# Performance work log

Measured on AMD Instinct MI355X. Metric: run time of the kernel, lower is better.

The kernel has to match this reference:

```python
import jax, jax.numpy as jnp
import numpy as np

T, B, NS, NC = 64, 128, 64, 32
NSC = NS + NC


def setup_inputs() -> dict:
    key = jax.random.key(0)
    k0, k1, k2, k3, k4, k5 = jax.random.split(key, 6)
    # SPD quadratic cost: C = L L^T + I  (mpc.pytorch requires Quu > 0)
    L = 0.1 * jax.random.normal(k0, (T, B, NSC, NSC), jnp.float32)
    C = jnp.einsum('tbij,tbkj->tbik', L, L) + jnp.eye(NSC, dtype=jnp.float32)
    c = jax.random.normal(k1, (T, B, NSC), jnp.float32)
    # Stable linear dynamics: x+ = Fx x + Fu u + f
    Fx = 0.95 * jnp.eye(NS, dtype=jnp.float32) + 0.02 * jax.random.normal(k2, (T, B, NS, NS), jnp.float32)
    Fu = 0.1 * jax.random.normal(k3, (T, B, NS, NC), jnp.float32)
    F = jnp.concatenate([Fx, Fu], axis=-1)
    f = 0.1 * jax.random.normal(k4, (T, B, NS), jnp.float32)
    x_init = jax.random.normal(k5, (B, NS), jnp.float32)
    return {"C": C, "c": c, "F": F, "f": f, "x_init": x_init}


def _lqr(C, c, F, f, x_init):
    """Exact batched time-varying LQR (Riccati backward pass + rollout).

    This is the math of MPC.solve_lqr_subproblem for LinDx/QuadCost with no
    control bounds; with quadratic cost & linear dynamics one iLQR iteration
    (alpha=1) is the exact solution.
    Returns tau = [x; u] trajectory, shape [T, B, NS+NC].
    """
    n = x_init.shape[-1]
    b = x_init.shape[0]
    dt = C.dtype

    def bwd(carry, inp):
        V, v = carry                      # V: [B,n,n], v: [B,n]
        Ct, ct, Ft, ft = inp
        # Q = C + F^T V F ; q = c + F^T (V f + v)
        Q = Ct + jnp.einsum('bsi,bst,btj->bij', Ft, V, Ft)
        q = ct + jnp.einsum('bsi,bs->bi', Ft, v + jnp.einsum('bst,bt->bs', V, ft))
        Qxx, Qxu = Q[:, :n, :n], Q[:, :n, n:]
        Qux, Quu = Q[:, n:, :n], Q[:, n:, n:]
        qx, qu = q[:, :n], q[:, n:]
        # One solve for both feedback gain K and feedforward k
        Kk = -jnp.linalg.solve(Quu, jnp.concatenate([Qux, qu[..., None]], axis=-1))
        K, k = Kk[..., :n], Kk[..., n]    # K: [B,nc,n], k: [B,nc]
        Vn = (Qxx
              + jnp.einsum('bim,bmj->bij', Qxu, K)
              + jnp.einsum('bmi,bmj->bij', K, Qux)
              + jnp.einsum('bmi,bmn,bnj->bij', K, Quu, K))
        Vn = 0.5 * (Vn + jnp.swapaxes(Vn, -1, -2))
        vn = (qx
              + jnp.einsum('bim,bm->bi', Qxu, k)
              + jnp.einsum('bmi,bm->bi', K, qu + jnp.einsum('bmn,bn->bm', Quu, k)))
        return (Vn, vn), (K, k)

    V0 = jnp.zeros((b, n, n), dt)
    v0 = jnp.zeros((b, n), dt)
    _, (Ks, ks) = jax.lax.scan(bwd, (V0, v0), (C, c, F, f), reverse=True)

    def fwd(x, inp):
        K, k, Ft, ft = inp
        u = jnp.einsum('bmi,bi->bm', K, x) + k
        tau = jnp.concatenate([x, u], axis=-1)
        x_next = jnp.einsum('bsi,bi->bs', Ft, tau) + ft
        return x_next, tau

    _, taus = jax.lax.scan(fwd, x_init, (Ks, ks, F, f))
    return taus  # [T, B, NSC]


def reference(C, c, F, f, x_init):
    return _lqr(C, c, F, f, x_init)
```

## Files before the change

kernel.cpp:

```cpp
#include <hip/hip_runtime.h>


constexpr int T_   = 64;
constexpr int B_   = 128;
constexpr int NS_  = 64;
constexpr int NC_  = 32;
constexpr int NSC_ = 96;

constexpr int OFF_VS   = 0;
constexpr int OFF_WS   = 4352;
constexpr int OFF_QU   = 10752;
constexpr int OFF_SS   = 13952;
constexpr int OFF_LT   = 18304;
constexpr int OFF_INVD = 20416;
constexpr int OFF_QV   = 20480;
constexpr int OFF_HV   = 20580;
constexpr int OFF_VV   = 20644;
constexpr int OFF_FB   = 20776;
constexpr int OFF_CU   = 33064;
constexpr int OFF_CF   = 36136;
constexpr int SMEM_F   = 37160;

typedef __attribute__((address_space(3))) void*       lds_vp;
typedef const __attribute__((address_space(1))) void* gas_vp;

__device__ __forceinline__ void g2l16(const float* g, float* l) {
  __builtin_amdgcn_global_load_lds((gas_vp)g, (lds_vp)l, 16, 0, 0);
}

__device__ __forceinline__ float rdlane(float v, int l) {
  return __builtin_bit_cast(float, __builtin_amdgcn_readlane(__builtin_bit_cast(int, v), l));
}

#define ASM_WAIT(S) asm volatile("s_waitcnt " S ::: "memory")
#define BAR()       __builtin_amdgcn_s_barrier()

__global__ __launch_bounds__(512) void lqr_all(
    const float* __restrict__ Cg, const float* __restrict__ cvg,
    const float* __restrict__ Fg, const float* __restrict__ fvg,
    const float* __restrict__ x0g, float* __restrict__ outg,
    float* __restrict__ Sws)
{
  const int b    = blockIdx.x;
  const int tid  = threadIdx.x;
  const int wid  = tid >> 6;
  const int lane = tid & 63;

  __shared__ float smem[SMEM_F];
  float (*Vs)[68]  = (float(*)[68]) (smem + OFF_VS);
  float (*Ws)[100] = (float(*)[100])(smem + OFF_WS);
  float (*Qu)[100] = (float(*)[100])(smem + OFF_QU);
  float* qv = smem + OFF_QV;
  float* hv = smem + OFF_HV;
  float* vv = smem + OFF_VV;

  for (int e = tid; e < 4352; e += 512) smem[e] = 0.f;
  if (tid < 64) vv[tid] = 0.f;

  const int b_r4 = (tid & 15) * 4;
  const int b_c4 = (tid >> 4) * 4;
  const int q_i0 = (tid / 24) * 4;
  const int q_j0 = (tid % 24) * 4;
  const int tvs  = tid - 192;
  const int v_r  = (tvs & 15) * 4;
  const int v_c  = ((tvs >> 4) & 15) * 4;
  const int tf2  = tid - 256;
  const int f_i  = ((tf2 >> 4) & 15) * 4;
  const int f_j  = (tf2 & 15) * 4;

  auto backsolve2 = [&](int pb, size_t tbn) {
    const int c = (tid - 128) >> 1;
    const int h = (tid - 128) & 1;
    const float (*Sp)[68]  = (const float(*)[68])(smem + OFF_SS + pb * 2176);
    const float (*LTp)[33] = (const float(*)[33])(smem + OFF_LT + pb * 1056);
    const float* ivp = smem + OFF_INVD + pb * 32;
    float r[16];
#pragma unroll
    for (int m = 0; m < 16; ++m) r[m] = Sp[2 * m + h][c];
    float* Sg = Sws + tbn * 2080;
#pragma unroll
    for (int k = 31; k >= 0; --k) {
      const float cand  = r[k >> 1] * ivp[k];
      const float other = __shfl_xor(cand, 1);
      const float xk = ((k & 1) == h) ? cand : other;
      if ((k & 1) == h) Sg[k * 65 + c] = xk;
#pragma unroll
      for (int m = 0; m <= (k - 1) >> 1; ++m) {
        if (h < k - 2 * m)
          r[m] -= LTp[2 * m + h][k] * xk;
      }
    }
  };

  {
    const size_t tb0 = (size_t)(T_ - 1) * B_ + b;
    if (wid == 7) {
      const int o = lane * 4;
      g2l16(cvg + tb0 * 96 + (o < 96 ? o : 92), smem + OFF_CF);
      g2l16(fvg + tb0 * 64 + (o < 64 ? o : 60), smem + OFF_CF + 256);
    }
    const float* Fbase = Fg + tb0 * (NS_ * NSC_);
#pragma unroll
    for (int r = 0; r < 3; ++r) {
      const int q = wid * 3 + r;
      g2l16(Fbase + q * 256 + lane * 4, smem + OFF_FB + q * 256);
    }
  }

  int cur = 0;

  for (int t = T_ - 1; t >= 0; --t) {
    const size_t tb = (size_t)t * B_ + b;
    float4 cxa0 = {}, cxa1 = {}, cxb0 = {}, cxb1 = {};

    {
      if (wid < 3) {
        const float* CuB = Cg + tb * 9216 + 64 * 96;
#pragma unroll
        for (int r = 0; r < 4; ++r) {
          const int q = wid * 4 + r;
          g2l16(CuB + q * 256 + lane * 4, smem + OFF_CU + q * 256);
        }
      } else if (wid < 7) {
        const float* Cb = Cg + tb * 9216;
        cxa0 = *(const float4*)(Cb + (v_r + 0) * 96 + v_c);
        cxa1 = *(const float4*)(Cb + (v_r + 1) * 96 + v_c);
        cxb0 = *(const float4*)(Cb + (v_r + 2) * 96 + v_c);
        cxb1 = *(const float4*)(Cb + (v_r + 3) * 96 + v_c);
      }
      const int tp = (t > 0) ? (t - 1) : 0;
      const size_t tbp = (size_t)tp * B_ + b;
      if (wid == 7) {
        float* cdst = smem + OFF_CF + (cur ^ 1) * 512;
        const int o = lane * 4;
        g2l16(cvg + tbp * 96 + (o < 96 ? o : 92), cdst);
        g2l16(fvg + tbp * 64 + (o < 64 ? o : 60), cdst + 256);
      }
      const float* Fbase = Fg + tbp * (NS_ * NSC_);
      float* fdst = smem + OFF_FB + (cur ^ 1) * 6144;
#pragma unroll
      for (int r = 0; r < 3; ++r) {
        const int q = wid * 3 + r;
        g2l16(Fbase + q * 256 + lane * 4, fdst + q * 256);
      }
    }

    if (wid == 7) { ASM_WAIT("vmcnt(5) lgkmcnt(0)"); }
    else         { ASM_WAIT("vmcnt(7) lgkmcnt(0)"); }
    BAR();

    const float* Fb = smem + OFF_FB + cur * 6144;
    const float* cf = smem + OFF_CF + cur * 512;

    if (tid < 384) {
      float acc[4][4];
#pragma unroll
      for (int a2 = 0; a2 < 4; ++a2)
#pragma unroll
        for (int j = 0; j < 4; ++j) acc[a2][j] = 0.f;
#pragma unroll 4
      for (int u = 0; u < 64; ++u) {
        const float4 va = *(const float4*)&Vs[u][b_r4];
        const float4 fb = *(const float4*)(Fb + u * 96 + b_c4);
        const float av[4] = {va.x, va.y, va.z, va.w};
        const float bv[4] = {fb.x, fb.y, fb.z, fb.w};
#pragma unroll
        for (int a2 = 0; a2 < 4; ++a2)
#pragma unroll
          for (int j = 0; j < 4; ++j) acc[a2][j] += av[a2] * bv[j];
      }
#pragma unroll
      for (int a2 = 0; a2 < 4; ++a2)
        *(float4*)&Ws[b_r4 + a2][b_c4] =
            make_float4(acc[a2][0], acc[a2][1], acc[a2][2], acc[a2][3]);
    } else if (tid < 448) {
      const int s = tid - 384;
      float acc = vv[s];
#pragma unroll
      for (int u4 = 0; u4 < 16; ++u4) {
        const float4 vr = *(const float4*)&Vs[s][u4 * 4];
        const float4 fr = *(const float4*)(cf + 256 + u4 * 4);
        acc += vr.x * fr.x + vr.y * fr.y + vr.z * fr.z + vr.w * fr.w;
      }
      hv[s] = acc;
    }

    ASM_WAIT("vmcnt(3) lgkmcnt(0)");
    BAR();

    if (tid < 192) {
      float a[4][4];
#pragma unroll
      for (int a2 = 0; a2 < 4; ++a2) {
        const float4 cu = *(const float4*)(smem + OFF_CU + (q_i0 + a2) * 96 + q_j0);
        a[a2][0] = cu.x; a[a2][1] = cu.y; a[a2][2] = cu.z; a[a2][3] = cu.w;
      }
#pragma unroll 4
      for (int u = 0; u < 64; ++u) {
        const float4 fu = *(const float4*)(Fb + u * 96 + 64 + q_i0);
        const float4 w4 = *(const float4*)&Ws[u][q_j0];
        const float av[4] = {fu.x, fu.y, fu.z, fu.w};
        const float wv[4] = {w4.x, w4.y, w4.z, w4.w};
#pragma unroll
        for (int a2 = 0; a2 < 4; ++a2)
#pragma unroll
          for (int j = 0; j < 4; ++j) a[a2][j] += av[a2] * wv[j];
      }
#pragma unroll
      for (int a2 = 0; a2 < 4; ++a2)
        *(float4*)&Qu[q_i0 + a2][q_j0] =
            make_float4(a[a2][0], a[a2][1], a[a2][2], a[a2][3]);
    } else if (tid < 448) {
      float a[4][4];
      a[0][0] = cxa0.x; a[0][1] = cxa0.y; a[0][2] = cxa0.z; a[0][3] = cxa0.w;
      a[1][0] = cxa1.x; a[1][1] = cxa1.y; a[1][2] = cxa1.z; a[1][3] = cxa1.w;
      a[2][0] = cxb0.x; a[2][1] = cxb0.y; a[2][2] = cxb0.z; a[2][3] = cxb0.w;
      a[3][0] = cxb1.x; a[3][1] = cxb1.y; a[3][2] = cxb1.z; a[3][3] = cxb1.w;
#pragma unroll 4
      for (int u = 0; u < 64; ++u) {
        const float4 fx = *(const float4*)(Fb + u * 96 + v_r);
        const float4 w4 = *(const float4*)&Ws[u][v_c];
        const float av[4] = {fx.x, fx.y, fx.z, fx.w};
        const float wv[4] = {w4.x, w4.y, w4.z, w4.w};
#pragma unroll
        for (int a2 = 0; a2 < 4; ++a2)
#pragma unroll
          for (int j = 0; j < 4; ++j) a[a2][j] += av[a2] * wv[j];
      }
#pragma unroll
      for (int a2 = 0; a2 < 4; ++a2)
        *(float4*)&Vs[v_r + a2][v_c] =
            make_float4(a[a2][0], a[a2][1], a[a2][2], a[a2][3]);
    } else {
      const int j = tid - 448;
      float acc0 = cf[j];
      float acc1 = (j < 32) ? cf[64 + j] : 0.f;
#pragma unroll 4
      for (int s2 = 0; s2 < 64; ++s2) {
        const float hs = hv[s2];
        acc0 += Fb[s2 * 96 + j] * hs;
        if (j < 32) acc1 += Fb[s2 * 96 + 64 + j] * hs;
      }
      qv[j] = acc0;
      if (j < 32) qv[64 + j] = acc1;
    }

    ASM_WAIT("lgkmcnt(0)");
    BAR();

    if (tid < 32) {
      const int i = tid;
      float a[32];
#pragma unroll
      for (int k = 0; k < 32; ++k) a[k] = Qu[i][64 + k];
      float (*LTc)[33] = (float(*)[33])(smem + OFF_LT + cur * 1056);
      float* ivc = smem + OFF_INVD + cur * 32;
#pragma unroll
      for (int j = 0; j < 32; ++j) {
        const float d   = rdlane(a[j], j);
        const float rin = 1.0f / sqrtf(d);
        const float l   = a[j] * rin;
        LTc[j][i] = l;
        if (i == 0) ivc[j] = rin;
#pragma unroll
        for (int k = j + 1; k < 32; ++k) {
          const float lkj = rdlane(l, k);
          a[k] = fmaf(-l, lkj, a[k]);
        }
      }
    }

    ASM_WAIT("lgkmcnt(0)");
    BAR();

    if (tid < 65) {
      const float (*LTc)[33] = (const float(*)[33])(smem + OFF_LT + cur * 1056);
      const float* ivc = smem + OFF_INVD + cur * 32;
      float r[32];
#pragma unroll
      for (int i2 = 0; i2 < 32; ++i2)
        r[i2] = (tid < 64) ? Qu[i2][tid] : qv[64 + i2];
#pragma unroll
      for (int i2 = 0; i2 < 32; ++i2) {
        const float yi = r[i2] * ivc[i2];
        r[i2] = yi;
#pragma unroll
        for (int k = i2 + 1; k < 32; ++k) r[k] -= LTc[i2][k] * yi;
      }
      float (*Sc)[68] = (float(*)[68])(smem + OFF_SS + cur * 2176);
#pragma unroll
      for (int i2 = 0; i2 < 32; ++i2) Sc[i2][tid] = r[i2];
    } else if (tid >= 128 && tid < 258) {
      if (t != T_ - 1) backsolve2(cur ^ 1, (size_t)(t + 1) * B_ + b);
    }

    ASM_WAIT("lgkmcnt(0)");
    BAR();

    {
      const float (*Sc)[68] = (const float(*)[68])(smem + OFF_SS + cur * 2176);
      if (tid >= 256) {
        float p[4][4];
#pragma unroll
        for (int a2 = 0; a2 < 4; ++a2)
#pragma unroll
          for (int j = 0; j < 4; ++j) p[a2][j] = 0.f;
#pragma unroll 4
        for (int m = 0; m < 32; ++m) {
          const float4 ya = *(const float4*)&Sc[m][f_i];
          const float4 yb = *(const float4*)&Sc[m][f_j];
          const float av[4] = {ya.x, ya.y, ya.z, ya.w};
          const float bv[4] = {yb.x, yb.y, yb.z, yb.w};
#pragma unroll
          for (int a2 = 0; a2 < 4; ++a2)
#pragma unroll
            for (int j = 0; j < 4; ++j) p[a2][j] += av[a2] * bv[j];
        }
#pragma unroll
        for (int a2 = 0; a2 < 4; ++a2) {
          float4 v4 = *(const float4*)&Vs[f_i + a2][f_j];
          v4.x -= p[a2][0]; v4.y -= p[a2][1]; v4.z -= p[a2][2]; v4.w -= p[a2][3];
          *(float4*)&Vs[f_i + a2][f_j] = v4;
        }
      } else if (tid < 64) {
        float acc = qv[tid];
#pragma unroll 4
        for (int m = 0; m < 32; ++m) acc -= Sc[m][tid] * Sc[m][64];
        vv[tid] = acc;
      }
    }
    cur ^= 1;
  }

  ASM_WAIT("vmcnt(0) lgkmcnt(0)");
  BAR();
  if (tid >= 128 && tid < 258) backsolve2(1, (size_t)b);
  ASM_WAIT("vmcnt(0) lgkmcnt(0)");
  BAR();

  float* tf = smem + OFF_QV;
  if (tid < 64) tf[tid] = x0g[(size_t)b * 64 + tid];

  auto stage_fwd = [&](int ts, int nb) {
    const size_t tbs = (size_t)ts * B_ + b;
    const float* Sb = Sws + tbs * 2080;
    float* sdst = smem + OFF_WS + nb * 2304;
#pragma unroll
    for (int r = 0; r < 2; ++r) {
      int q = wid * 2 + r; if (q > 8) q = 8;
      const int off = q * 256 + lane * 4;
      g2l16(Sb + (off < 2080 ? off : 2076), sdst + q * 256);
    }
    const float* Fbase = Fg + tbs * (NS_ * NSC_);
    float* fdst = smem + OFF_FB + nb * 6144;
#pragma unroll
    for (int r = 0; r < 3; ++r) {
      const int q = wid * 3 + r;
      g2l16(Fbase + q * 256 + lane * 4, fdst + q * 256);
    }
    const int o = lane * 4;
    g2l16(fvg + tbs * 64 + (o < 64 ? o : 60), smem + OFF_CF + nb * 512);
  };

  stage_fwd(0, 0);
  cur = 0;
  const int s4 = tid >> 2, l4 = tid & 3;
  for (int t = 0; t < T_; ++t) {
    const size_t tb = (size_t)t * B_ + b;
    stage_fwd((t < T_ - 1) ? t + 1 : T_ - 1, cur ^ 1);
    ASM_WAIT("vmcnt(6) lgkmcnt(0)");
    BAR();

    const float* Fbc = smem + OFF_FB + cur * 6144;
    float ax = 0.f;

    if (tid < 64) outg[tb * 96 + tid] = tf[tid];
    if (tid < 256) {
      const float* Fr = Fbc + s4 * 96 + l4 * 16;
#pragma unroll
      for (int q = 0; q < 4; ++q) {
        const float4 fq = *(const float4*)(Fr + q * 4);
        const float4 xq = *(const float4*)&tf[l4 * 16 + q * 4];
        ax += fq.x * xq.x + fq.y * xq.y + fq.z * xq.z + fq.w * xq.w;
      }
    } else {
      const int m = (tid - 256) >> 3, l8 = tid & 7;
      const float* Sr = smem + OFF_WS + cur * 2304 + m * 65;
      float p = (l8 == 0) ? Sr[64] : 0.f;
      const int i0 = l8 * 8;
#pragma unroll
      for (int ii = 0; ii < 8; ++ii) p += Sr[i0 + ii] * tf[i0 + ii];
      p += __shfl_xor(p, 1); p += __shfl_xor(p, 2); p += __shfl_xor(p, 4);
      if (l8 == 0) tf[64 + m] = -p;
    }
    ASM_WAIT("lgkmcnt(0)");
    BAR();

    if (tid < 256) {
      const float* Fu = Fbc + s4 * 96 + 64 + l4 * 8;
      const float4 g0 = *(const float4*)(Fu);
      const float4 g1 = *(const float4*)(Fu + 4);
      const float4 u0 = *(const float4*)&tf[64 + l4 * 8];
      const float4 u1 = *(const float4*)&tf[64 + l4 * 8 + 4];
      float p = ax + g0.x * u0.x + g0.y * u0.y + g0.z * u0.z + g0.w * u0.w
                   + g1.x * u1.x + g1.y * u1.y + g1.z * u1.z + g1.w * u1.w;
      p += __shfl_xor(p, 1); p += __shfl_xor(p, 2);
      if (l4 == 0) tf[s4] = p + *(smem + OFF_CF + cur * 512 + s4);
    } else if (tid < 288) {
      const int m = tid - 256;
      outg[tb * 96 + 64 + m] = tf[64 + m];
    }
    ASM_WAIT("lgkmcnt(0)");
    BAR();
    cur ^= 1;
  }
}

extern "C" void kernel_launch(void* const* d_in, const int* in_sizes, int n_in,
                              void* d_out, int out_size, void* d_ws, size_t ws_size,
                              hipStream_t stream) {
  const float* C  = (const float*)d_in[0];
  const float* c  = (const float*)d_in[1];
  const float* F  = (const float*)d_in[2];
  const float* f  = (const float*)d_in[3];
  const float* x0 = (const float*)d_in[4];
  float* out = (float*)d_out;
  float* S   = (float*)d_ws;

  lqr_all<<<dim3(B_), dim3(512), 0, stream>>>(C, c, F, f, x0, out, S);
}
```

Baseline: 1.756 ms.

## Use packed FP32 FMA in GEMM loops, load Cu into registers, overlap backsolve with Cholesky

Rewrites the 4x4 register-tile inner loops of the V·F, F^T·W and Schur-update products with inline-asm v_pk_fma_f32, so each instruction performs two FMAs. The Cuu block of C is now read straight into registers by waves 0-2 instead of being staged through LDS. This drops one LDS buffer and relaxes a vmcnt wait. The backsolve of the previous step moves into the same phase as the Cholesky factorisation, which gets raised wave priority, so the two run concurrently. The inline asm bypasses compiler scheduling, and the register-loaded C adds latency exposure before the second barrier.

Measured after the change: 1.690 ms. 3.8% less time.

```diff
diff --git a/kernel.cpp b/kernel.cpp
--- a/kernel.cpp
+++ b/kernel.cpp
@@ -17,9 +17,11 @@
 constexpr int OFF_HV   = 20580;
 constexpr int OFF_VV   = 20644;
 constexpr int OFF_FB   = 20776;
-constexpr int OFF_CU   = 33064;
-constexpr int OFF_CF   = 36136;
-constexpr int SMEM_F   = 37160;
+constexpr int OFF_CF   = 33064;
+constexpr int SMEM_F   = 34088;
+
+typedef __attribute__((ext_vector_type(2))) float f32x2;
+typedef __attribute__((ext_vector_type(4))) float f32x4;
 
 typedef __attribute__((address_space(3))) void*       lds_vp;
 typedef const __attribute__((address_space(1))) void* gas_vp;
@@ -30,6 +32,21 @@
 
 __device__ __forceinline__ float rdlane(float v, int l) {
   return __builtin_bit_cast(float, __builtin_amdgcn_readlane(__builtin_bit_cast(int, v), l));
+}
+
+__device__ __forceinline__ void pk_lo(f32x2& d, f32x2 a, f32x2 b) {
+  asm("v_pk_fma_f32 %0, %1, %2, %0 op_sel:[0,0,0] op_sel_hi:[1,0,1]"
+      : "+v"(d) : "v"(a), "v"(b));
+}
+__device__ __forceinline__ void pk_hi(f32x2& d, f32x2 a, f32x2 b) {
+  asm("v_pk_fma_f32 %0, %1, %2, %0 op_sel:[0,1,0] op_sel_hi:[1,1,1]"
+      : "+v"(d) : "v"(a), "v"(b));
+}
+
+__device__ __forceinline__ f32x4 ld4(const float* p) { return *(const f32x4*)p; }
+__device__ __forceinline__ void st4(float* p, float x, float y, float z, float w) {
+  f32x4 v = {x, y, z, w};
+  *(f32x4*)p = v;
 }
 
 #define ASM_WAIT(S) asm volatile("s_waitcnt " S ::: "memory")
@@ -111,22 +128,17 @@
 
   for (int t = T_ - 1; t >= 0; --t) {
     const size_t tb = (size_t)t * B_ + b;
-    float4 cxa0 = {}, cxa1 = {}, cxb0 = {}, cxb1 = {};
+
+    f32x4 c0 = {0, 0, 0, 0}, c1 = {0, 0, 0, 0}, c2 = {0, 0, 0, 0}, c3 = {0, 0, 0, 0};
 
     {
+      const float* Cb = Cg + tb * 9216;
       if (wid < 3) {
-        const float* CuB = Cg + tb * 9216 + 64 * 96;
-#pragma unroll
-        for (int r = 0; r < 4; ++r) {
-          const int q = wid * 4 + r;
-          g2l16(CuB + q * 256 + lane * 4, smem + OFF_CU + q * 256);
-        }
+        const float* cp = Cb + (64 + q_i0) * 96 + q_j0;
+        c0 = ld4(cp); c1 = ld4(cp + 96); c2 = ld4(cp + 192); c3 = ld4(cp + 288);
       } else if (wid < 7) {
-        const float* Cb = Cg + tb * 9216;
-        cxa0 = *(const float4*)(Cb + (v_r + 0) * 96 + v_c);
-        cxa1 = *(const float4*)(Cb + (v_r + 1) * 96 + v_c);
-        cxb0 = *(const float4*)(Cb + (v_r + 2) * 96 + v_c);
-        cxb1 = *(const float4*)(Cb + (v_r + 3) * 96 + v_c);
+        const float* cp = Cb + v_r * 96 + v_c;
+        c0 = ld4(cp); c1 = ld4(cp + 96); c2 = ld4(cp + 192); c3 = ld4(cp + 288);
       }
       const int tp = (t > 0) ? (t - 1) : 0;
       const size_t tbp = (size_t)tp * B_ + b;
@@ -153,84 +165,71 @@
     const float* cf = smem + OFF_CF + cur * 512;
 
     if (tid < 384) {
-      float acc[4][4];
-#pragma unroll
-      for (int a2 = 0; a2 < 4; ++a2)
-#pragma unroll
-        for (int j = 0; j < 4; ++j) acc[a2][j] = 0.f;
+      f32x2 a00 = {0, 0}, a01 = {0, 0}, a02 = {0, 0}, a03 = {0, 0};
+      f32x2 a10 = {0, 0}, a11 = {0, 0}, a12 = {0, 0}, a13 = {0, 0};
 #pragma unroll 4
       for (int u = 0; u < 64; ++u) {
-        const float4 va = *(const float4*)&Vs[u][b_r4];
-        const float4 fb = *(const float4*)(Fb + u * 96 + b_c4);
-        const float av[4] = {va.x, va.y, va.z, va.w};
-        const float bv[4] = {fb.x, fb.y, fb.z, fb.w};
-#pragma unroll
-        for (int a2 = 0; a2 < 4; ++a2)
-#pragma unroll
-          for (int j = 0; j < 4; ++j) acc[a2][j] += av[a2] * bv[j];
-      }
-#pragma unroll
-      for (int a2 = 0; a2 < 4; ++a2)
-        *(float4*)&Ws[b_r4 + a2][b_c4] =
-            make_float4(acc[a2][0], acc[a2][1], acc[a2][2], acc[a2][3]);
+        const f32x4 va = ld4(&Vs[u][b_r4]);
+        const f32x4 fb = ld4(Fb + u * 96 + b_c4);
+        const f32x2 vl = va.lo, vh = va.hi, bl = fb.lo, bh = fb.hi;
+        pk_lo(a00, vl, bl); pk_hi(a01, vl, bl);
+        pk_lo(a02, vl, bh); pk_hi(a03, vl, bh);
+        pk_lo(a10, vh, bl); pk_hi(a11, vh, bl);
+        pk_lo(a12, vh, bh); pk_hi(a13, vh, bh);
+      }
+      st4(&Ws[b_r4 + 0][b_c4], a00.x, a01.x, a02.x, a03.x);
+      st4(&Ws[b_r4 + 1][b_c4], a00.y, a01.y, a02.y, a03.y);
+      st4(&Ws[b_r4 + 2][b_c4], a10.x, a11.x, a12.x, a13.x);
+      st4(&Ws[b_r4 + 3][b_c4], a10.y, a11.y, a12.y, a13.y);
     } else if (tid < 448) {
       const int s = tid - 384;
       float acc = vv[s];
 #pragma unroll
       for (int u4 = 0; u4 < 16; ++u4) {
-        const float4 vr = *(const float4*)&Vs[s][u4 * 4];
-        const float4 fr = *(const float4*)(cf + 256 + u4 * 4);
+        const f32x4 vr = ld4(&Vs[s][u4 * 4]);
+        const f32x4 fr = ld4(cf + 256 + u4 * 4);
         acc += vr.x * fr.x + vr.y * fr.y + vr.z * fr.z + vr.w * fr.w;
       }
       hv[s] = acc;
     }
 
-    ASM_WAIT("vmcnt(3) lgkmcnt(0)");
+    ASM_WAIT("lgkmcnt(0)");
     BAR();
 
     if (tid < 192) {
-      float a[4][4];
-#pragma unroll
-      for (int a2 = 0; a2 < 4; ++a2) {
-        const float4 cu = *(const float4*)(smem + OFF_CU + (q_i0 + a2) * 96 + q_j0);
-        a[a2][0] = cu.x; a[a2][1] = cu.y; a[a2][2] = cu.z; a[a2][3] = cu.w;
-      }
+      f32x2 a00 = {c0.x, c1.x}, a01 = {c0.y, c1.y}, a02 = {c0.z, c1.z}, a03 = {c0.w, c1.w};
+      f32x2 a10 = {c2.x, c3.x}, a11 = {c2.y, c3.y}, a12 = {c2.z, c3.z}, a13 = {c2.w, c3.w};
 #pragma unroll 4
       for (int u = 0; u < 64; ++u) {
-        const float4 fu = *(const float4*)(Fb + u * 96 + 64 + q_i0);
-        const float4 w4 = *(const float4*)&Ws[u][q_j0];
-        const float av[4] = {fu.x, fu.y, fu.z, fu.w};
-        const float wv[4] = {w4.x, w4.y, w4.z, w4.w};
-#pragma unroll
-        for (int a2 = 0; a2 < 4; ++a2)
-#pragma unroll
-          for (int j = 0; j < 4; ++j) a[a2][j] += av[a2] * wv[j];
-      }
-#pragma unroll
-      for (int a2 = 0; a2 < 4; ++a2)
-        *(float4*)&Qu[q_i0 + a2][q_j0] =
-            make_float4(a[a2][0], a[a2][1], a[a2][2], a[a2][3]);
+        const f32x4 fu = ld4(Fb + u * 96 + 64 + q_i0);
+        const f32x4 w4 = ld4(&Ws[u][q_j0]);
+        const f32x2 al = fu.lo, ah = fu.hi, bl = w4.lo, bh = w4.hi;
+        pk_lo(a00, al, bl); pk_hi(a01, al, bl);
+        pk_lo(a02, al, bh); pk_hi(a03, al, bh);
+        pk_lo(a10, ah, bl); pk_hi(a11, ah, bl);
+        pk_lo(a12, ah, bh); pk_hi(a13, ah, bh);
+      }
+      st4(&Qu[q_i0 + 0][q_j0], a00.x, a01.x, a02.x, a03.x);
+      st4(&Qu[q_i0 + 1][q_j0], a00.y, a01.y, a02.y, a03.y);
+      st4(&Qu[q_i0 + 2][q_j0], a10.x, a11.x, a12.x, a13.x);
+      st4(&Qu[q_i0 + 3][q_j0], a10.y, a11.y, a12.y, a13.y);
     } else if (tid < 448) {
-      float a[4][4];
-      a[0][0] = cxa0.x; a[0][1] = cxa0.y; a[0][2] = cxa0.z; a[0][3] = cxa0.w;
-      a[1][0] = cxa1.x; a[1][1] = cxa1.y; a[1][2] = cxa1.z; a[1][3] = cxa1.w;
-      a[2][0] = cxb0.x; a[2][1] = cxb0.y; a[2][2] = cxb0.z; a[2][3] = cxb0.w;
-      a[3][0] = cxb1.x; a[3][1] = cxb1.y; a[3][2] = cxb1.z; a[3][3] = cxb1.w;
+      f32x2 a00 = {c0.x, c1.x}, a01 = {c0.y, c1.y}, a02 = {c0.z, c1.z}, a03 = {c0.w, c1.w};
+      f32x2 a10 = {c2.x, c3.x}, a11 = {c2.y, c3.y}, a12 = {c2.z, c3.z}, a13 = {c2.w, c3.w};
 #pragma unroll 4
       for (int u = 0; u < 64; ++u) {
-        const float4 fx = *(const float4*)(Fb + u * 96 + v_r);
-        const float4 w4 = *(const float4*)&Ws[u][v_c];
-        const float av[4] = {fx.x, fx.y, fx.z, fx.w};
-        const float wv[4] = {w4.x, w4.y, w4.z, w4.w};
-#pragma unroll
-        for (int a2 = 0; a2 < 4; ++a2)
-#pragma unroll
-          for (int j = 0; j < 4; ++j) a[a2][j] += av[a2] * wv[j];
-      }
-#pragma unroll
-      for (int a2 = 0; a2 < 4; ++a2)
-        *(float4*)&Vs[v_r + a2][v_c] =
-            make_float4(a[a2][0], a[a2][1], a[a2][2], a[a2][3]);
+        const f32x4 fx = ld4(Fb + u * 96 + v_r);
+        const f32x4 w4 = ld4(&Ws[u][v_c]);
+        const f32x2 al = fx.lo, ah = fx.hi, bl = w4.lo, bh = w4.hi;
+        pk_lo(a00, al, bl); pk_hi(a01, al, bl);
+        pk_lo(a02, al, bh); pk_hi(a03, al, bh);
+        pk_lo(a10, ah, bl); pk_hi(a11, ah, bl);
+        pk_lo(a12, ah, bh); pk_hi(a13, ah, bh);
+      }
+      st4(&Vs[v_r + 0][v_c], a00.x, a01.x, a02.x, a03.x);
+      st4(&Vs[v_r + 1][v_c], a00.y, a01.y, a02.y, a03.y);
+      st4(&Vs[v_r + 2][v_c], a10.x, a11.x, a12.x, a13.x);
+      st4(&Vs[v_r + 3][v_c], a10.y, a11.y, a12.y, a13.y);
     } else {
       const int j = tid - 448;
       float acc0 = cf[j];
@@ -249,6 +248,7 @@
     BAR();
 
     if (tid < 32) {
+      __builtin_amdgcn_s_setprio(1);
       const int i = tid;
       float a[32];
 #pragma unroll
@@ -268,6 +268,9 @@
           a[k] = fmaf(-l, lkj, a[k]);
         }
       }
+      __builtin_amdgcn_s_setprio(0);
+    } else if (tid >= 128 && tid < 258) {
+      if (t != T_ - 1) backsolve2(cur ^ 1, (size_t)(t + 1) * B_ + b);
     }
 
     ASM_WAIT("lgkmcnt(0)");
@@ -290,8 +293,6 @@
       float (*Sc)[68] = (float(*)[68])(smem + OFF_SS + cur * 2176);
 #pragma unroll
       for (int i2 = 0; i2 < 32; ++i2) Sc[i2][tid] = r[i2];
-    } else if (tid >= 128 && tid < 258) {
-      if (t != T_ - 1) backsolve2(cur ^ 1, (size_t)(t + 1) * B_ + b);
     }
 
     ASM_WAIT("lgkmcnt(0)");
@@ -300,28 +301,26 @@
     {
       const float (*Sc)[68] = (const float(*)[68])(smem + OFF_SS + cur * 2176);
       if (tid >= 256) {
-        float p[4][4];
-#pragma unroll
-        for (int a2 = 0; a2 < 4; ++a2)
-#pragma unroll
-          for (int j = 0; j < 4; ++j) p[a2][j] = 0.f;
+        f32x2 p00 = {0, 0}, p01 = {0, 0}, p02 = {0, 0}, p03 = {0, 0};
+        f32x2 p10 = {0, 0}, p11 = {0, 0}, p12 = {0, 0}, p13 = {0, 0};
 #pragma unroll 4
         for (int m = 0; m < 32; ++m) {
-          const float4 ya = *(const float4*)&Sc[m][f_i];
-          const float4 yb = *(const float4*)&Sc[m][f_j];
-          const float av[4] = {ya.x, ya.y, ya.z, ya.w};
-          const float bv[4] = {yb.x, yb.y, yb.z, yb.w};
-#pragma unroll
-          for (int a2 = 0; a2 < 4; ++a2)
-#pragma unroll
-            for (int j = 0; j < 4; ++j) p[a2][j] += av[a2] * bv[j];
+          const f32x4 ya = ld4(&Sc[m][f_i]);
+          const f32x4 yb = ld4(&Sc[m][f_j]);
+          const f32x2 al = ya.lo, ah = ya.hi, bl = yb.lo, bh = yb.hi;
+          pk_lo(p00, al, bl); pk_hi(p01, al, bl);
+          pk_lo(p02, al, bh); pk_hi(p03, al, bh);
+          pk_lo(p10, ah, bl); pk_hi(p11, ah, bl);
+          pk_lo(p12, ah, bh); pk_hi(p13, ah, bh);
         }
-#pragma unroll
-        for (int a2 = 0; a2 < 4; ++a2) {
-          float4 v4 = *(const float4*)&Vs[f_i + a2][f_j];
-          v4.x -= p[a2][0]; v4.y -= p[a2][1]; v4.z -= p[a2][2]; v4.w -= p[a2][3];
-          *(float4*)&Vs[f_i + a2][f_j] = v4;
-        }
+        f32x4 v0 = ld4(&Vs[f_i + 0][f_j]);
+        f32x4 v1 = ld4(&Vs[f_i + 1][f_j]);
+        f32x4 v2 = ld4(&Vs[f_i + 2][f_j]);
+        f32x4 v3 = ld4(&Vs[f_i + 3][f_j]);
+        st4(&Vs[f_i + 0][f_j], v0.x - p00.x, v0.y - p01.x, v0.z - p02.x, v0.w - p03.x);
+        st4(&Vs[f_i + 1][f_j], v1.x - p00.y, v1.y - p01.y, v1.z - p02.y, v1.w - p03.y);
+        st4(&Vs[f_i + 2][f_j], v2.x - p10.x, v2.y - p11.x, v2.z - p12.x, v2.w - p13.x);
+        st4(&Vs[f_i + 3][f_j], v3.x - p10.y, v3.y - p11.y, v3.z - p12.y, v3.w - p13.y);
       } else if (tid < 64) {
         float acc = qv[tid];
 #pragma unroll 4
@@ -379,8 +378,8 @@
       const float* Fr = Fbc + s4 * 96 + l4 * 16;
 #pragma unroll
       for (int q = 0; q < 4; ++q) {
-        const float4 fq = *(const float4*)(Fr + q * 4);
-        const float4 xq = *(const float4*)&tf[l4 * 16 + q * 4];
+        const f32x4 fq = ld4(Fr + q * 4);
+        const f32x4 xq = ld4(&tf[l4 * 16 + q * 4]);
         ax += fq.x * xq.x + fq.y * xq.y + fq.z * xq.z + fq.w * xq.w;
       }
     } else {
@@ -398,10 +397,10 @@
 
     if (tid < 256) {
       const float* Fu = Fbc + s4 * 96 + 64 + l4 * 8;
-      const float4 g0 = *(const float4*)(Fu);
-      const float4 g1 = *(const float4*)(Fu + 4);
-      const float4 u0 = *(const float4*)&tf[64 + l4 * 8];
-      const float4 u1 = *(const float4*)&tf[64 + l4 * 8 + 4];
+      const f32x4 g0 = ld4(Fu);
+      const f32x4 g1 = ld4(Fu + 4);
+      const f32x4 u0 = ld4(&tf[64 + l4 * 8]);
+      const f32x4 u1 = ld4(&tf[64 + l4 * 8 + 4]);
       float p = ax + g0.x * u0.x + g0.y * u0.y + g0.z * u0.z + g0.w * u0.w
                    + g1.x * u1.x + g1.y * u1.y + g1.z * u1.z + g1.w * u1.w;
       p += __shfl_xor(p, 1); p += __shfl_xor(p, 2);
```
